# Kernel optimization log

Measured on AMD Instinct MI355X. Metric: run time of the kernel, lower is better.

The kernel has to match this reference:

```python
import jax, jax.numpy as jnp
import numpy as np

N = 100_000          # nodes
E = 1_600_000        # directed edges (avg degree 16)
H = 128              # hidden_dim
OUT = 5              # output_dim (actions)
FOV = 11             # input_dim -> image side
LIN_IN = (FOV - 2) ** 2 * 3  # 243
LN_EPS = 1e-5


def _conv2d(x, w, b):
    # x: [N,3,h,w], w: [3,3,3,3] OIHW, VALID, stride 1
    y = jax.lax.conv_general_dilated(
        x, w, window_strides=(1, 1), padding='VALID',
        dimension_numbers=('NCHW', 'OIHW', 'NCHW'))
    return y + b[None, :, None, None]


def setup_inputs() -> dict:
    key = jax.random.key(0)
    ks = jax.random.split(key, 32)
    r = lambda i, shape, s=0.05: (jax.random.normal(ks[i], shape, jnp.float32) * s)
    inp = {
        'x': jax.random.normal(ks[0], (N, 3, FOV, FOV), jnp.float32),
        'edge_index': jax.random.randint(ks[1], (2, E), 0, N, jnp.int64)
                      if jax.config.jax_enable_x64 else
                      jax.random.randint(ks[1], (2, E), 0, N, jnp.int32),
        # CustomConv params
        'conv_w': r(2, (3, 3, 3, 3)), 'conv_b': r(3, (3,)),
        'conv_self_w': r(4, (3, 3, 3, 3)), 'conv_self_b': r(5, (3,)),
        'lin_w': r(6, (LIN_IN, H)), 'lin_b': r(7, (H,)),
        'lin_self_w': r(8, (LIN_IN, H)), 'lin_self_b': r(9, (H,)),
        # 3 SAGEConv layers: lin_l (aggregated, with bias), lin_r (root, no bias)
        'sage_lw': r(10, (3, H, H)), 'sage_lb': r(11, (3, H)),
        'sage_rw': r(12, (3, H, H)),
        # LayerNorms applied after layers 0,1,2
        'ln_g': jnp.ones((3, H), jnp.float32), 'ln_b': jnp.zeros((3, H), jnp.float32),
        # post_mp MLP (dropout is identity in eval)
        'mlp_w1': r(13, (H, H)), 'mlp_b1': r(14, (H,)),
        'mlp_w2': r(15, (H, OUT)), 'mlp_b2': r(16, (OUT,)),
    }
    return inp


def _layernorm(h, g, b):
    mu = jnp.mean(h, axis=-1, keepdims=True)
    var = jnp.var(h, axis=-1, keepdims=True)
    return (h - mu) * jax.lax.rsqrt(var + LN_EPS) * g + b


def reference(x, edge_index, conv_w, conv_b, conv_self_w, conv_self_b,
              lin_w, lin_b, lin_self_w, lin_self_b,
              sage_lw, sage_lb, sage_rw, ln_g, ln_b,
              mlp_w1, mlp_b1, mlp_w2, mlp_b2):
    src, dst = edge_index[0], edge_index[1]
    valid = (src != dst)  # remove_self_loops (CustomConv only)

    # ---- layer 0: CustomConv (add aggregation) ----
    self_x = jax.nn.relu(_conv2d(x, conv_self_w, conv_self_b).reshape(N, -1))
    self_x = self_x @ lin_self_w + lin_self_b              # [N,H]
    xn = jax.nn.relu(_conv2d(x, conv_w, conv_b).reshape(N, -1))
    xn = xn @ lin_w + lin_b                                # [N,H]
    msgs = xn[src] * valid[:, None].astype(xn.dtype)       # gather + mask self loops
    h = self_x + jax.ops.segment_sum(msgs, dst, num_segments=N)

    # SAGE mean-degree counts (all edges; SAGE does not remove self loops)
    cnt = jnp.maximum(
        jax.ops.segment_sum(jnp.ones((E,), h.dtype), dst, num_segments=N), 1.0)

    emb = h
    for i in range(4):
        if i > 0:
            j = i - 1
            agg = jax.ops.segment_sum(h[src], dst, num_segments=N) / cnt[:, None]
            h = agg @ sage_lw[j] + sage_lb[j] + h @ sage_rw[j]
        emb = h
        h = jax.nn.relu(h)            # dropout p=0.25 is identity in eval
        if i != 3:
            h = _layernorm(h, ln_g[i], ln_b[i])

    # task == 'node': no pooling
    logits = (h @ mlp_w1 + mlp_b1) @ mlp_w2 + mlp_b2
    return emb, jax.nn.log_softmax(logits, axis=1)
```

## Files before the change

kernel.cpp:

```cpp
#include <hip/hip_runtime.h>
#include <hip/hip_bf16.h>

typedef __hip_bfloat16 bf16;
typedef __attribute__((ext_vector_type(8))) short v8s;
typedef __attribute__((ext_vector_type(4))) float v4f;

#define N_NODES 100000
#define N_EDGES 1600000
#define LN_EPS 1e-5f

#define OFF_CONV_W      0
#define OFF_CONV_B      81
#define OFF_CONV_SW     84
#define OFF_CONV_SB     165
#define OFF_LIN_W       168
#define OFF_LIN_B       31272
#define OFF_LIN_SW      31400
#define OFF_LIN_SB      62504
#define OFF_SAGE_LW     62632
#define OFF_SAGE_LB     111784
#define OFF_SAGE_RW     112168
#define OFF_LN_G        161320
#define OFF_LN_B        161704
#define OFF_MLP_W1      162088
#define OFF_MLP_B1      178472
#define OFF_MLP_W2      178600
#define OFF_MLP_B2      179240
#define PARAM_TOTAL     179245

#define WTL_N 65536
#define WTS_N 98304
#define WTM_N 16384

__device__ __forceinline__ unsigned short f2b(float f) {
    bf16 h = __float2bfloat16(f);
    return __builtin_bit_cast(unsigned short, h);
}
__device__ __forceinline__ float blo(unsigned u) { return __uint_as_float(u << 16); }
__device__ __forceinline__ float bhi(unsigned u) { return __uint_as_float(u & 0xffff0000u); }
__device__ __forceinline__ unsigned pack2(float lo, float hi) {
    return (unsigned)f2b(lo) | ((unsigned)f2b(hi) << 16);
}

struct Ptr17 { const void* p[17]; };

__global__ void detect_kernel(const unsigned short* __restrict__ xw,
                              const unsigned int* __restrict__ ew,
                              int* __restrict__ flags) {
    __shared__ int sawBigExp, sawHigh;
    if (threadIdx.x == 0) { sawBigExp = 0; sawHigh = 0; }
    __syncthreads();
    int localBig = 0, localHigh = 0;
    for (int i = threadIdx.x; i < 65536; i += 256) {
        unsigned e = (xw[i] >> 7) & 0xFF;
        if (e >= 0xF0) localBig = 1;
    }
    for (int i = threadIdx.x; i < 8192; i += 256) {
        if (ew[2 * i + 1] != 0) localHigh = 1;
    }
    if (localBig) atomicOr(&sawBigExp, 1);
    if (localHigh) atomicOr(&sawHigh, 1);
    __syncthreads();
    if (threadIdx.x == 0) { flags[0] = sawBigExp; flags[1] = sawHigh ? 0 : 1; }
}

__global__ void cvt_params_kernel(Ptr17 ptrs, const int* __restrict__ flags,
                                  float* __restrict__ dst) {
    int i = blockIdx.x * 256 + threadIdx.x;
    if (i >= PARAM_TOTAL) return;
    const int ksz[17] = {81,3,81,3,31104,128,31104,128,49152,384,49152,384,384,16384,128,640,5};
    int seg = 0, off = i;
    while (off >= ksz[seg]) { off -= ksz[seg]; ++seg; }
    float v;
    if (flags[0]) v = ((const float*)ptrs.p[seg])[off];
    else          v = __bfloat162float(((const bf16*)ptrs.p[seg])[off]);
    dst[i] = v;
}

__global__ void cvt2_kernel(const float* __restrict__ P,
                            unsigned short* __restrict__ wtl,
                            unsigned short* __restrict__ wts,
                            unsigned short* __restrict__ wtm) {
    int i = blockIdx.x * 256 + threadIdx.x;
    if (i < WTL_N) {
        int f = i >> 8, k = i & 255;
        float v = 0.f;
        if (k < 243) v = (f < 128) ? P[OFF_LIN_W + k * 128 + f]
                                   : P[OFF_LIN_SW + k * 128 + (f - 128)];
        wtl[i] = f2b(v);
    } else if (i < WTL_N + WTS_N) {
        int j = i - WTL_N; int l = j >> 15; int r = j & 32767; int f = r >> 8; int k = r & 255;
        float v = (k < 128) ? P[OFF_SAGE_LW + l * 16384 + k * 128 + f]
                            : P[OFF_SAGE_RW + l * 16384 + (k - 128) * 128 + f];
        wts[j] = f2b(v);
    } else if (i < WTL_N + WTS_N + WTM_N) {
        int j = i - WTL_N - WTS_N; int f = j >> 7, k = j & 127;
        wtm[j] = f2b(P[OFF_MLP_W1 + k * 128 + f]);
    }
}

__global__ __launch_bounds__(320) void conv_lin_kernel(
    const void* __restrict__ x, const float* __restrict__ P,
    const unsigned short* __restrict__ wtl, const int* __restrict__ flags,
    unsigned short* __restrict__ xnb, float* __restrict__ selfh)
{
    __shared__ unsigned short xs[5808];
    __shared__ unsigned short ysb[16][2][256];
    __shared__ float wc[2][81];
    __shared__ float bc[2][3];
    int tid = threadIdx.x;
    int n0 = blockIdx.x * 16;

    if (tid < 81) { wc[0][tid] = P[OFF_CONV_W + tid]; wc[1][tid] = P[OFF_CONV_SW + tid]; }
    else if (tid < 84) { int o = tid - 81; bc[0][o] = P[OFF_CONV_B + o]; bc[1][o] = P[OFF_CONV_SB + o]; }

    for (int i = tid; i < 416; i += 320) {
        int j = i / 26, r2 = i % 26, p = r2 / 13, k = 243 + (r2 % 13);
        ysb[j][p][k] = 0;
    }

    if (flags[0]) {
        const float* xf = (const float*)x + (size_t)n0 * 363;
        for (int i = tid; i < 5808; i += 320) xs[i] = f2b(xf[i]);
    } else {
        const uint4* xsrc = (const uint4*)((const unsigned short*)x + (size_t)n0 * 363);
        uint4* xd = (uint4*)xs;
        for (int i = tid; i < 726; i += 320) xd[i] = xsrc[i];
    }
    __syncthreads();

    if (tid < 288) {
        int j = tid / 18, rem = tid % 18;
        int p = rem / 9, oi = rem % 9;
        float acc[27];
        #pragma unroll
        for (int o = 0; o < 3; o++) {
            float b = bc[p][o];
            #pragma unroll
            for (int oj = 0; oj < 9; oj++) acc[o * 9 + oj] = b;
        }
        #pragma unroll
        for (int c = 0; c < 3; c++) {
            #pragma unroll
            for (int ki = 0; ki < 3; ki++) {
                float xr[11];
                const unsigned short* row = &xs[j * 363 + c * 121 + (oi + ki) * 11];
                #pragma unroll
                for (int t = 0; t < 11; t++) xr[t] = blo(row[t]);
                #pragma unroll
                for (int o = 0; o < 3; o++) {
                    int wb = o * 27 + c * 9 + ki * 3;
                    float w0 = wc[p][wb], w1 = wc[p][wb + 1], w2 = wc[p][wb + 2];
                    #pragma unroll
                    for (int oj = 0; oj < 9; oj++)
                        acc[o * 9 + oj] += xr[oj] * w0 + xr[oj + 1] * w1 + xr[oj + 2] * w2;
                }
            }
        }
        #pragma unroll
        for (int o = 0; o < 3; o++)
            #pragma unroll
            for (int oj = 0; oj < 9; oj++)
                ysb[j][p][o * 81 + oi * 9 + oj] = f2b(fmaxf(acc[o * 9 + oj], 0.f));
    }
    __syncthreads();

    int wave = tid >> 6, lane = tid & 63, quad = lane >> 4, col = lane & 15;
    if (wave < 4) {
        int p = wave >> 1;
        v4f acc[4];
        #pragma unroll
        for (int t = 0; t < 4; t++) { acc[t][0] = 0.f; acc[t][1] = 0.f; acc[t][2] = 0.f; acc[t][3] = 0.f; }
        for (int s = 0; s < 8; s++) {
            int kq = s * 32 + quad * 8;
            v8s a = *(const v8s*)&ysb[col][p][kq];
            #pragma unroll
            for (int t = 0; t < 4; t++) {
                int f = (wave * 4 + t) * 16 + col;
                v8s b = *(const v8s*)&wtl[(size_t)f * 256 + kq];
                acc[t] = __builtin_amdgcn_mfma_f32_16x16x32_bf16(a, b, acc[t], 0, 0, 0);
            }
        }
        #pragma unroll
        for (int t = 0; t < 4; t++) {
            int f = (wave * 4 + t) * 16 + col;
            #pragma unroll
            for (int r = 0; r < 4; r++) {
                int node = n0 + quad * 4 + r;
                float v = acc[t][r];
                if (p == 0) xnb[(size_t)node * 128 + f] = f2b(v + P[OFF_LIN_B + f]);
                else        selfh[(size_t)node * 128 + (f - 128)] = v + P[OFF_LIN_SB + (f - 128)];
            }
        }
    }
}

__device__ __forceinline__ int ld_edge(const int* __restrict__ ew, size_t elem, int isi64) {
    size_t idx = isi64 ? (elem * 2) : elem;
    return ew[idx];
}

__global__ void degree_kernel(const int* __restrict__ ew, const int* __restrict__ flags,
                              int* __restrict__ deg) {
    int e = blockIdx.x * blockDim.x + threadIdx.x;
    if (e < N_EDGES) {
        int d = ld_edge(ew, (size_t)N_EDGES + e, flags[1]);
        if ((unsigned)d < N_NODES) atomicAdd(&deg[d], 1);
    }
}

__global__ __launch_bounds__(1024) void scanA(const int* __restrict__ deg, int* __restrict__ rowptr,
                                              float* __restrict__ cntf, int* __restrict__ bsum) {
    __shared__ int s[1024];
    int tid = threadIdx.x;
    int i = blockIdx.x * 1024 + tid;
    int v = (i < N_NODES) ? deg[i] : 0;
    s[tid] = v;
    __syncthreads();
    for (int off = 1; off < 1024; off <<= 1) {
        int t = (tid >= off) ? s[tid - off] : 0;
        __syncthreads();
        s[tid] += t;
        __syncthreads();
    }
    if (i < N_NODES) {
        rowptr[i] = s[tid] - v;
        cntf[i] = (float)(v < 1 ? 1 : v);
    }
    if (tid == 1023) bsum[blockIdx.x] = s[1023];
}

__global__ void scanB(const int* __restrict__ bsum, int* __restrict__ boff, int nb, int* __restrict__ rowptr_end) {
    if (threadIdx.x == 0 && blockIdx.x == 0) {
        int run = 0;
        for (int i = 0; i < nb; i++) { boff[i] = run; run += bsum[i]; }
        *rowptr_end = run;
    }
}

__global__ __launch_bounds__(1024) void scanC(int* __restrict__ rowptr, const int* __restrict__ boff,
                                              int* __restrict__ cursor) {
    int i = blockIdx.x * 1024 + threadIdx.x;
    if (i < N_NODES) {
        int v = rowptr[i] + boff[blockIdx.x];
        rowptr[i] = v;
        cursor[i] = v;
    }
}

__global__ void fill_kernel(const int* __restrict__ ew, const int* __restrict__ flags,
                            int* __restrict__ cursor, int* __restrict__ csr) {
    int e = blockIdx.x * blockDim.x + threadIdx.x;
    if (e < N_EDGES) {
        int isi64 = flags[1];
        int s = ld_edge(ew, (size_t)e, isi64);
        int d = ld_edge(ew, (size_t)N_EDGES + e, isi64);
        if ((unsigned)d < N_NODES) {
            int p = atomicAdd(&cursor[d], 1);
            if ((unsigned)p < N_EDGES)
                csr[p] = ((unsigned)s < N_NODES) ? (s | ((s == d) ? (int)0x80000000 : 0)) : -1;
        }
    }
}

__global__ __launch_bounds__(256) void agg0ln_kernel(const unsigned short* __restrict__ xnb,
        const float* __restrict__ selfh, const int* __restrict__ rowptr, const int* __restrict__ csr,
        const float* __restrict__ lng, const float* __restrict__ lnb,
        unsigned short* __restrict__ zb) {
    int wave = threadIdx.x >> 6, lane = threadIdx.x & 63;
    int g = lane >> 4, c = lane & 15;
    int n = blockIdx.x * 4 + wave;
    int beg = rowptr[n], end = rowptr[n + 1];
    float a[8];
    #pragma unroll
    for (int i = 0; i < 8; i++) a[i] = 0.f;
    const uint4* x4 = (const uint4*)xnb;
    for (int b = beg; b < end; b += 64) {
        int bl = b + lane;
        int my = (bl < end) ? csr[bl] : -1;
        int nb = end - b; if (nb > 64) nb = 64;
        for (int i = 0; i < nb; i += 16) {
            int sv0 = __shfl(my, i + g, 64);
            int sv1 = __shfl(my, i + 4 + g, 64);
            int sv2 = __shfl(my, i + 8 + g, 64);
            int sv3 = __shfl(my, i + 12 + g, 64);
            bool va0 = ((unsigned)sv0 < N_NODES);
            bool va1 = ((unsigned)sv1 < N_NODES);
            bool va2 = ((unsigned)sv2 < N_NODES);
            bool va3 = ((unsigned)sv3 < N_NODES);
            uint4 v0 = x4[(size_t)(va0 ? sv0 : 0) * 16 + c];
            uint4 v1 = x4[(size_t)(va1 ? sv1 : 0) * 16 + c];
            uint4 v2 = x4[(size_t)(va2 ? sv2 : 0) * 16 + c];
            uint4 v3 = x4[(size_t)(va3 ? sv3 : 0) * 16 + c];
            if (va0) {
                a[0] += blo(v0.x); a[1] += bhi(v0.x);
                a[2] += blo(v0.y); a[3] += bhi(v0.y);
                a[4] += blo(v0.z); a[5] += bhi(v0.z);
                a[6] += blo(v0.w); a[7] += bhi(v0.w);
            }
            if (va1) {
                a[0] += blo(v1.x); a[1] += bhi(v1.x);
                a[2] += blo(v1.y); a[3] += bhi(v1.y);
                a[4] += blo(v1.z); a[5] += bhi(v1.z);
                a[6] += blo(v1.w); a[7] += bhi(v1.w);
            }
            if (va2) {
                a[0] += blo(v2.x); a[1] += bhi(v2.x);
                a[2] += blo(v2.y); a[3] += bhi(v2.y);
                a[4] += blo(v2.z); a[5] += bhi(v2.z);
                a[6] += blo(v2.w); a[7] += bhi(v2.w);
            }
            if (va3) {
                a[0] += blo(v3.x); a[1] += bhi(v3.x);
                a[2] += blo(v3.y); a[3] += bhi(v3.y);
                a[4] += blo(v3.z); a[5] += bhi(v3.z);
                a[6] += blo(v3.w); a[7] += bhi(v3.w);
            }
        }
    }
    #pragma unroll
    for (int i = 0; i < 8; i++) {
        a[i] += __shfl_xor(a[i], 16, 64);
        a[i] += __shfl_xor(a[i], 32, 64);
    }
    if (g == 0) {
        const float4* s4 = (const float4*)(selfh + (size_t)n * 128 + c * 8);
        float4 s0 = s4[0], s1 = s4[1];
        float v[8];
        v[0] = s0.x + a[0]; v[1] = s0.y + a[1]; v[2] = s0.z + a[2]; v[3] = s0.w + a[3];
        v[4] = s1.x + a[4]; v[5] = s1.y + a[5]; v[6] = s1.z + a[6]; v[7] = s1.w + a[7];
        float s = 0.f, sq = 0.f;
        #pragma unroll
        for (int i = 0; i < 8; i++) {
            v[i] = fmaxf(v[i], 0.f);
            s += v[i]; sq += v[i] * v[i];
        }
        #pragma unroll
        for (int m = 8; m >= 1; m >>= 1) {
            s  += __shfl_xor(s, m, 64);
            sq += __shfl_xor(sq, m, 64);
        }
        float mu = s * (1.f / 128.f);
        float var = sq * (1.f / 128.f) - mu * mu;
        float is = rsqrtf(var + LN_EPS);
        const float4* g4 = (const float4*)(lng + c * 8);
        const float4* b4 = (const float4*)(lnb + c * 8);
        float4 g0 = g4[0], g1 = g4[1], b0 = b4[0], b1 = b4[1];
        float z[8];
        z[0] = (v[0] - mu) * is * g0.x + b0.x; z[1] = (v[1] - mu) * is * g0.y + b0.y;
        z[2] = (v[2] - mu) * is * g0.z + b0.z; z[3] = (v[3] - mu) * is * g0.w + b0.w;
        z[4] = (v[4] - mu) * is * g1.x + b1.x; z[5] = (v[5] - mu) * is * g1.y + b1.y;
        z[6] = (v[6] - mu) * is * g1.z + b1.z; z[7] = (v[7] - mu) * is * g1.w + b1.w;
        uint4 o;
        o.x = pack2(z[0], z[1]); o.y = pack2(z[2], z[3]);
        o.z = pack2(z[4], z[5]); o.w = pack2(z[6], z[7]);
        ((uint4*)zb)[(size_t)n * 16 + c] = o;
    }
}

__global__ __launch_bounds__(256) void aggm_kernel(const unsigned short* __restrict__ zb,
        const int* __restrict__ rowptr, const int* __restrict__ csr,
        const float* __restrict__ cntf, unsigned short* __restrict__ aggb) {
    int wave = threadIdx.x >> 6, lane = threadIdx.x & 63;
    int g = lane >> 4, c = lane & 15;
    int n = blockIdx.x * 4 + wave;
    int beg = rowptr[n], end = rowptr[n + 1];
    float a[8];
    #pragma unroll
    for (int i = 0; i < 8; i++) a[i] = 0.f;
    const uint4* z4 = (const uint4*)zb;
    for (int b = beg; b < end; b += 64) {
        int bl = b + lane;
        int my = (bl < end) ? csr[bl] : -1;
        int nb = end - b; if (nb > 64) nb = 64;
        for (int i = 0; i < nb; i += 16) {
            int sv0 = __shfl(my, i + g, 64) & 0x7fffffff;
            int sv1 = __shfl(my, i + 4 + g, 64) & 0x7fffffff;
            int sv2 = __shfl(my, i + 8 + g, 64) & 0x7fffffff;
            int sv3 = __shfl(my, i + 12 + g, 64) & 0x7fffffff;
            bool va0 = (sv0 < N_NODES);
            bool va1 = (sv1 < N_NODES);
            bool va2 = (sv2 < N_NODES);
            bool va3 = (sv3 < N_NODES);
            uint4 v0 = z4[(size_t)(va0 ? sv0 : 0) * 16 + c];
            uint4 v1 = z4[(size_t)(va1 ? sv1 : 0) * 16 + c];
            uint4 v2 = z4[(size_t)(va2 ? sv2 : 0) * 16 + c];
            uint4 v3 = z4[(size_t)(va3 ? sv3 : 0) * 16 + c];
            if (va0) {
                a[0] += blo(v0.x); a[1] += bhi(v0.x);
                a[2] += blo(v0.y); a[3] += bhi(v0.y);
                a[4] += blo(v0.z); a[5] += bhi(v0.z);
                a[6] += blo(v0.w); a[7] += bhi(v0.w);
            }
            if (va1) {
                a[0] += blo(v1.x); a[1] += bhi(v1.x);
                a[2] += blo(v1.y); a[3] += bhi(v1.y);
                a[4] += blo(v1.z); a[5] += bhi(v1.z);
                a[6] += blo(v1.w); a[7] += bhi(v1.w);
            }
            if (va2) {
                a[0] += blo(v2.x); a[1] += bhi(v2.x);
                a[2] += blo(v2.y); a[3] += bhi(v2.y);
                a[4] += blo(v2.z); a[5] += bhi(v2.z);
                a[6] += blo(v2.w); a[7] += bhi(v2.w);
            }
            if (va3) {
                a[0] += blo(v3.x); a[1] += bhi(v3.x);
                a[2] += blo(v3.y); a[3] += bhi(v3.y);
                a[4] += blo(v3.z); a[5] += bhi(v3.z);
                a[6] += blo(v3.w); a[7] += bhi(v3.w);
            }
        }
    }
    #pragma unroll
    for (int i = 0; i < 8; i++) {
        a[i] += __shfl_xor(a[i], 16, 64);
        a[i] += __shfl_xor(a[i], 32, 64);
    }
    if (g == 0) {
        float inv = 1.f / cntf[n];
        uint4 o;
        o.x = pack2(a[0] * inv, a[1] * inv); o.y = pack2(a[2] * inv, a[3] * inv);
        o.z = pack2(a[4] * inv, a[5] * inv); o.w = pack2(a[6] * inv, a[7] * inv);
        ((uint4*)aggb)[(size_t)n * 16 + c] = o;
    }
}

__global__ __launch_bounds__(256) void sageln_kernel(const unsigned short* __restrict__ aggb,
        unsigned short* __restrict__ zb, const unsigned short* __restrict__ wts,
        const float* __restrict__ lb, const float* __restrict__ lng, const float* __restrict__ lnb,
        int last, float* __restrict__ hout) {
    __shared__ float hb[16][128];
    int tid = threadIdx.x;
    int n0 = blockIdx.x * 16;
    int wave = tid >> 6, lane = tid & 63, quad = lane >> 4, col = lane & 15;
    int nodeA = n0 + col;

    v4f acc[2];
    #pragma unroll
    for (int t = 0; t < 2; t++) { acc[t][0] = 0.f; acc[t][1] = 0.f; acc[t][2] = 0.f; acc[t][3] = 0.f; }
    #pragma unroll
    for (int s = 0; s < 8; s++) {
        int kq = s * 32 + quad * 8;
        const unsigned short* abase = (s < 4) ? (aggb + (size_t)nodeA * 128 + kq)
                                              : (zb + (size_t)nodeA * 128 + (kq - 128));
        v8s a = *(const v8s*)abase;
        #pragma unroll
        for (int t = 0; t < 2; t++) {
            int f = (wave * 2 + t) * 16 + col;
            v8s b = *(const v8s*)&wts[(size_t)f * 256 + kq];
            acc[t] = __builtin_amdgcn_mfma_f32_16x16x32_bf16(a, b, acc[t], 0, 0, 0);
        }
    }
    #pragma unroll
    for (int t = 0; t < 2; t++) {
        int f = (wave * 2 + t) * 16 + col;
        float bias = lb[f];
        #pragma unroll
        for (int r = 0; r < 4; r++)
            hb[quad * 4 + r][f] = acc[t][r] + bias;
    }
    __syncthreads();

    #pragma unroll
    for (int jj = 0; jj < 4; jj++) {
        int j = wave * 4 + jj;
        int node = n0 + j;
        float v0 = hb[j][2 * lane], v1 = hb[j][2 * lane + 1];
        if (last) {
            float2 w; w.x = v0; w.y = v1;
            ((float2*)hout)[(size_t)node * 64 + lane] = w;
        } else {
            float r0 = fmaxf(v0, 0.f), r1 = fmaxf(v1, 0.f);
            float s = r0 + r1, sq = r0 * r0 + r1 * r1;
            #pragma unroll
            for (int m = 32; m >= 1; m >>= 1) {
                s  += __shfl_xor(s, m, 64);
                sq += __shfl_xor(sq, m, 64);
            }
            float mu = s * (1.f / 128.f);
            float var = sq * (1.f / 128.f) - mu * mu;
            float inv = rsqrtf(var + LN_EPS);
            float z0 = (r0 - mu) * inv * lng[2 * lane]     + lnb[2 * lane];
            float z1 = (r1 - mu) * inv * lng[2 * lane + 1] + lnb[2 * lane + 1];
            ((unsigned int*)zb)[(size_t)node * 64 + lane] = pack2(z0, z1);
        }
    }
}

__global__ __launch_bounds__(256) void mlp_kernel(const float* __restrict__ h,
        const unsigned short* __restrict__ wtm, const float* __restrict__ P,
        const int* __restrict__ flags, void* __restrict__ out) {
    __shared__ unsigned short rb[16][128];
    __shared__ float mb[16][128];
    __shared__ float lg[16][5];
    int tid = threadIdx.x;
    int n0 = blockIdx.x * 16;
    int isf = flags[0];

    const float2* h2 = (const float2*)h;
    for (int i = tid; i < 16 * 64; i += 256) {
        int j = i >> 6, q = i & 63;
        float2 v = h2[(size_t)(n0 + j) * 64 + q];
        size_t oi = (size_t)(n0 + j) * 128 + 2 * q;
        if (isf) { ((float*)out)[oi] = v.x; ((float*)out)[oi + 1] = v.y; }
        else ((unsigned int*)out)[oi >> 1] = pack2(v.x, v.y);
        rb[j][2 * q]     = f2b(fmaxf(v.x, 0.f));
        rb[j][2 * q + 1] = f2b(fmaxf(v.y, 0.f));
    }
    __syncthreads();

    int wave = tid >> 6, lane = tid & 63, quad = lane >> 4, col = lane & 15;
    v4f acc[2];
    #pragma unroll
    for (int t = 0; t < 2; t++) { acc[t][0] = 0.f; acc[t][1] = 0.f; acc[t][2] = 0.f; acc[t][3] = 0.f; }
    #pragma unroll
    for (int s = 0; s < 4; s++) {
        int kq = s * 32 + quad * 8;
        v8s a = *(const v8s*)&rb[col][kq];
        #pragma unroll
        for (int t = 0; t < 2; t++) {
            int f = (wave * 2 + t) * 16 + col;
            v8s b = *(const v8s*)&wtm[(size_t)f * 128 + kq];
            acc[t] = __builtin_amdgcn_mfma_f32_16x16x32_bf16(a, b, acc[t], 0, 0, 0);
        }
    }
    #pragma unroll
    for (int t = 0; t < 2; t++) {
        int f = (wave * 2 + t) * 16 + col;
        float bias = P[OFF_MLP_B1 + f];
        #pragma unroll
        for (int r = 0; r < 4; r++)
            mb[quad * 4 + r][f] = acc[t][r] + bias;
    }
    __syncthreads();

    if (tid < 80) {
        int j = tid / 5, o = tid - (tid / 5) * 5;
        float a = P[OFF_MLP_B2 + o];
        for (int k = 0; k < 128; k++) a += mb[j][k] * P[OFF_MLP_W2 + k * 5 + o];
        lg[j][o] = a;
    }
    __syncthreads();
    if (tid < 16) {
        int j = tid;
        float mx = lg[j][0];
        #pragma unroll
        for (int o = 1; o < 5; o++) mx = fmaxf(mx, lg[j][o]);
        float se = 0.f;
        #pragma unroll
        for (int o = 0; o < 5; o++) se += expf(lg[j][o] - mx);
        float lse = mx + logf(se);
        size_t base = (size_t)N_NODES * 128 + (size_t)(n0 + j) * 5;
        #pragma unroll
        for (int o = 0; o < 5; o++) {
            float v = lg[j][o] - lse;
            if (isf) ((float*)out)[base + o] = v;
            else     ((bf16*)out)[base + o] = __float2bfloat16(v);
        }
    }
}

extern "C" void kernel_launch(void* const* d_in, const int* in_sizes, int n_in,
                              void* d_out, int out_size, void* d_ws, size_t ws_size,
                              hipStream_t stream) {
    const void* x  = d_in[0];
    const int*  ew = (const int*)d_in[1];

    Ptr17 ptrs;
    for (int i = 0; i < 17; i++) ptrs.p[i] = d_in[2 + i];

    char* w = (char*)d_ws;
    auto carve = [&](size_t bytes) { char* r = w; w += (bytes + 255) & ~(size_t)255; return r; };
    float*          bufS  = (float*)carve((size_t)N_NODES * 128 * 4);
    unsigned short* xnb   = (unsigned short*)carve((size_t)N_NODES * 128 * 2);
    unsigned short* zb    = (unsigned short*)carve((size_t)N_NODES * 128 * 2);
    unsigned short* aggb  = (unsigned short*)carve((size_t)N_NODES * 128 * 2);
    float*          pf32  = (float*)carve((size_t)PARAM_TOTAL * 4);
    unsigned short* wtl   = (unsigned short*)carve((size_t)WTL_N * 2);
    unsigned short* wts   = (unsigned short*)carve((size_t)WTS_N * 2);
    unsigned short* wtm   = (unsigned short*)carve((size_t)WTM_N * 2);
    int*   deg    = (int*)carve((size_t)N_NODES * 4);
    int*   rowptr = (int*)carve((size_t)(N_NODES + 64) * 4);
    int*   cursor = (int*)carve((size_t)N_NODES * 4);
    float* cntf   = (float*)carve((size_t)N_NODES * 4);
    int*   bsum   = (int*)carve(512);
    int*   boff   = (int*)carve(512);
    int*   flags  = (int*)carve(256);
    int*   csr    = (int*)carve((size_t)N_EDGES * 4);

    const int SCAN_BLOCKS = (N_NODES + 1023) / 1024;

    detect_kernel<<<1, 256, 0, stream>>>((const unsigned short*)x, (const unsigned int*)ew, flags);
    cvt_params_kernel<<<(PARAM_TOTAL + 255) / 256, 256, 0, stream>>>(ptrs, flags, pf32);
    cvt2_kernel<<<(WTL_N + WTS_N + WTM_N + 255) / 256, 256, 0, stream>>>(pf32, wtl, wts, wtm);

    hipMemsetAsync(deg, 0, (size_t)N_NODES * 4, stream);

    conv_lin_kernel<<<N_NODES / 16, 320, 0, stream>>>(x, pf32, wtl, flags, xnb, bufS);

    degree_kernel<<<(N_EDGES + 255) / 256, 256, 0, stream>>>(ew, flags, deg);
    scanA<<<SCAN_BLOCKS, 1024, 0, stream>>>(deg, rowptr, cntf, bsum);
    scanB<<<1, 1, 0, stream>>>(bsum, boff, SCAN_BLOCKS, rowptr + N_NODES);
    scanC<<<SCAN_BLOCKS, 1024, 0, stream>>>(rowptr, boff, cursor);
    fill_kernel<<<(N_EDGES + 255) / 256, 256, 0, stream>>>(ew, flags, cursor, csr);

    agg0ln_kernel<<<N_NODES / 4, 256, 0, stream>>>(xnb, bufS, rowptr, csr,
        pf32 + OFF_LN_G, pf32 + OFF_LN_B, zb);

    for (int l = 0; l < 3; l++) {
        aggm_kernel<<<N_NODES / 4, 256, 0, stream>>>(zb, rowptr, csr, cntf, aggb);
        sageln_kernel<<<N_NODES / 16, 256, 0, stream>>>(aggb, zb, wts + (size_t)l * 32768,
            pf32 + OFF_SAGE_LB + l * 128,
            pf32 + OFF_LN_G + (l + 1) * 128, pf32 + OFF_LN_B + (l + 1) * 128,
            (l == 2) ? 1 : 0, bufS);
    }

    mlp_kernel<<<N_NODES / 16, 256, 0, stream>>>(bufS, wtm, pf32, flags, d_out);
}
```

Baseline: 1.150 ms.

## Fuse SAGE mean-aggregation into the MFMA linear+LayerNorm kernel with ping-pong buffers

Merges the neighbor mean-aggregation kernel and the SAGE linear+LayerNorm kernel into one. Each block aggregates 16 nodes into shared memory, then feeds them straight to the MFMA. The next layer's activations go to a separate ping-pong buffer, so other blocks never see an overwritten input. This removes one launch per layer and the global write and reread of the aggregated features. In exchange, the block does its gathers serially per wave (4 nodes each) before the MFMA, and the MFMA loads now mix LDS and global reads, which could hurt latency hiding.

Result: faster. 1.087 ms (-5.5%).

```diff
diff --git a/kernel.cpp b/kernel.cpp
--- a/kernel.cpp
+++ b/kernel.cpp
@@ -358,92 +358,95 @@
     }
 }
 
-__global__ __launch_bounds__(256) void aggm_kernel(const unsigned short* __restrict__ zb,
+__global__ __launch_bounds__(256) void sagefused_kernel(
+        const unsigned short* __restrict__ cur,
         const int* __restrict__ rowptr, const int* __restrict__ csr,
-        const float* __restrict__ cntf, unsigned short* __restrict__ aggb) {
-    int wave = threadIdx.x >> 6, lane = threadIdx.x & 63;
-    int g = lane >> 4, c = lane & 15;
-    int n = blockIdx.x * 4 + wave;
-    int beg = rowptr[n], end = rowptr[n + 1];
-    float a[8];
-    #pragma unroll
-    for (int i = 0; i < 8; i++) a[i] = 0.f;
-    const uint4* z4 = (const uint4*)zb;
-    for (int b = beg; b < end; b += 64) {
-        int bl = b + lane;
-        int my = (bl < end) ? csr[bl] : -1;
-        int nb = end - b; if (nb > 64) nb = 64;
-        for (int i = 0; i < nb; i += 16) {
-            int sv0 = __shfl(my, i + g, 64) & 0x7fffffff;
-            int sv1 = __shfl(my, i + 4 + g, 64) & 0x7fffffff;
-            int sv2 = __shfl(my, i + 8 + g, 64) & 0x7fffffff;
-            int sv3 = __shfl(my, i + 12 + g, 64) & 0x7fffffff;
-            bool va0 = (sv0 < N_NODES);
-            bool va1 = (sv1 < N_NODES);
-            bool va2 = (sv2 < N_NODES);
-            bool va3 = (sv3 < N_NODES);
-            uint4 v0 = z4[(size_t)(va0 ? sv0 : 0) * 16 + c];
-            uint4 v1 = z4[(size_t)(va1 ? sv1 : 0) * 16 + c];
-            uint4 v2 = z4[(size_t)(va2 ? sv2 : 0) * 16 + c];
-            uint4 v3 = z4[(size_t)(va3 ? sv3 : 0) * 16 + c];
-            if (va0) {
-                a[0] += blo(v0.x); a[1] += bhi(v0.x);
-                a[2] += blo(v0.y); a[3] += bhi(v0.y);
-                a[4] += blo(v0.z); a[5] += bhi(v0.z);
-                a[6] += blo(v0.w); a[7] += bhi(v0.w);
-            }
-            if (va1) {
-                a[0] += blo(v1.x); a[1] += bhi(v1.x);
-                a[2] += blo(v1.y); a[3] += bhi(v1.y);
-                a[4] += blo(v1.z); a[5] += bhi(v1.z);
-                a[6] += blo(v1.w); a[7] += bhi(v1.w);
-            }
-            if (va2) {
-                a[0] += blo(v2.x); a[1] += bhi(v2.x);
-                a[2] += blo(v2.y); a[3] += bhi(v2.y);
-                a[4] += blo(v2.z); a[5] += bhi(v2.z);
-                a[6] += blo(v2.w); a[7] += bhi(v2.w);
-            }
-            if (va3) {
-                a[0] += blo(v3.x); a[1] += bhi(v3.x);
-                a[2] += blo(v3.y); a[3] += bhi(v3.y);
-                a[4] += blo(v3.z); a[5] += bhi(v3.z);
-                a[6] += blo(v3.w); a[7] += bhi(v3.w);
-            }
-        }
-    }
-    #pragma unroll
-    for (int i = 0; i < 8; i++) {
-        a[i] += __shfl_xor(a[i], 16, 64);
-        a[i] += __shfl_xor(a[i], 32, 64);
-    }
-    if (g == 0) {
-        float inv = 1.f / cntf[n];
-        uint4 o;
-        o.x = pack2(a[0] * inv, a[1] * inv); o.y = pack2(a[2] * inv, a[3] * inv);
-        o.z = pack2(a[4] * inv, a[5] * inv); o.w = pack2(a[6] * inv, a[7] * inv);
-        ((uint4*)aggb)[(size_t)n * 16 + c] = o;
-    }
-}
-
-__global__ __launch_bounds__(256) void sageln_kernel(const unsigned short* __restrict__ aggb,
-        unsigned short* __restrict__ zb, const unsigned short* __restrict__ wts,
+        const float* __restrict__ cntf, const unsigned short* __restrict__ wts,
         const float* __restrict__ lb, const float* __restrict__ lng, const float* __restrict__ lnb,
-        int last, float* __restrict__ hout) {
+        int last, unsigned short* __restrict__ nxt, float* __restrict__ hout) {
+    __shared__ unsigned short al[16][128];
     __shared__ float hb[16][128];
     int tid = threadIdx.x;
     int n0 = blockIdx.x * 16;
-    int wave = tid >> 6, lane = tid & 63, quad = lane >> 4, col = lane & 15;
+    int wave = tid >> 6, lane = tid & 63;
+    int g = lane >> 4, c = lane & 15;
+    const uint4* z4 = (const uint4*)cur;
+
+    for (int q = 0; q < 4; q++) {
+        int jj = wave * 4 + q;
+        int n = n0 + jj;
+        int beg = rowptr[n], end = rowptr[n + 1];
+        float a[8];
+        #pragma unroll
+        for (int i = 0; i < 8; i++) a[i] = 0.f;
+        for (int b = beg; b < end; b += 64) {
+            int bl = b + lane;
+            int my = (bl < end) ? csr[bl] : -1;
+            int nb = end - b; if (nb > 64) nb = 64;
+            for (int i = 0; i < nb; i += 16) {
+                int sv0 = __shfl(my, i + g, 64) & 0x7fffffff;
+                int sv1 = __shfl(my, i + 4 + g, 64) & 0x7fffffff;
+                int sv2 = __shfl(my, i + 8 + g, 64) & 0x7fffffff;
+                int sv3 = __shfl(my, i + 12 + g, 64) & 0x7fffffff;
+                bool va0 = (sv0 < N_NODES);
+                bool va1 = (sv1 < N_NODES);
+                bool va2 = (sv2 < N_NODES);
+                bool va3 = (sv3 < N_NODES);
+                uint4 v0 = z4[(size_t)(va0 ? sv0 : 0) * 16 + c];
+                uint4 v1 = z4[(size_t)(va1 ? sv1 : 0) * 16 + c];
+                uint4 v2 = z4[(size_t)(va2 ? sv2 : 0) * 16 + c];
+                uint4 v3 = z4[(size_t)(va3 ? sv3 : 0) * 16 + c];
+                if (va0) {
+                    a[0] += blo(v0.x); a[1] += bhi(v0.x);
+                    a[2] += blo(v0.y); a[3] += bhi(v0.y);
+                    a[4] += blo(v0.z); a[5] += bhi(v0.z);
+                    a[6] += blo(v0.w); a[7] += bhi(v0.w);
+                }
+                if (va1) {
+                    a[0] += blo(v1.x); a[1] += bhi(v1.x);
+                    a[2] += blo(v1.y); a[3] += bhi(v1.y);
+                    a[4] += blo(v1.z); a[5] += bhi(v1.z);
+                    a[6] += blo(v1.w); a[7] += bhi(v1.w);
+                }
+                if (va2) {
+                    a[0] += blo(v2.x); a[1] += bhi(v2.x);
+                    a[2] += blo(v2.y); a[3] += bhi(v2.y);
+                    a[4] += blo(v2.z); a[5] += bhi(v2.z);
+                    a[6] += blo(v2.w); a[7] += bhi(v2.w);
+                }
+                if (va3) {
+                    a[0] += blo(v3.x); a[1] += bhi(v3.x);
+                    a[2] += blo(v3.y); a[3] += bhi(v3.y);
+                    a[4] += blo(v3.z); a[5] += bhi(v3.z);
+                    a[6] += blo(v3.w); a[7] += bhi(v3.w);
+                }
+            }
+        }
+        #pragma unroll
+        for (int i = 0; i < 8; i++) {
+            a[i] += __shfl_xor(a[i], 16, 64);
+            a[i] += __shfl_xor(a[i], 32, 64);
+        }
+        if (g == 0) {
+            float inv = 1.f / cntf[n];
+            uint4 o;
+            o.x = pack2(a[0] * inv, a[1] * inv); o.y = pack2(a[2] * inv, a[3] * inv);
+            o.z = pack2(a[4] * inv, a[5] * inv); o.w = pack2(a[6] * inv, a[7] * inv);
+            ((uint4*)&al[jj][0])[c] = o;
+        }
+    }
+    __syncthreads();
+
+    int quad = g, col = c;
     int nodeA = n0 + col;
-
     v4f acc[2];
     #pragma unroll
     for (int t = 0; t < 2; t++) { acc[t][0] = 0.f; acc[t][1] = 0.f; acc[t][2] = 0.f; acc[t][3] = 0.f; }
     #pragma unroll
     for (int s = 0; s < 8; s++) {
         int kq = s * 32 + quad * 8;
-        const unsigned short* abase = (s < 4) ? (aggb + (size_t)nodeA * 128 + kq)
-                                              : (zb + (size_t)nodeA * 128 + (kq - 128));
+        const unsigned short* abase = (s < 4) ? &al[col][kq]
+                                              : (cur + (size_t)nodeA * 128 + (kq - 128));
         v8s a = *(const v8s*)abase;
         #pragma unroll
         for (int t = 0; t < 2; t++) {
@@ -483,7 +486,7 @@
             float inv = rsqrtf(var + LN_EPS);
             float z0 = (r0 - mu) * inv * lng[2 * lane]     + lnb[2 * lane];
             float z1 = (r1 - mu) * inv * lng[2 * lane + 1] + lnb[2 * lane + 1];
-            ((unsigned int*)zb)[(size_t)node * 64 + lane] = pack2(z0, z1);
+            ((unsigned int*)nxt)[(size_t)node * 64 + lane] = pack2(z0, z1);
         }
     }
 }
@@ -608,12 +611,15 @@
     agg0ln_kernel<<<N_NODES / 4, 256, 0, stream>>>(xnb, bufS, rowptr, csr,
         pf32 + OFF_LN_G, pf32 + OFF_LN_B, zb);
 
+    unsigned short* cur = zb;
+    unsigned short* nxt = aggb;
     for (int l = 0; l < 3; l++) {
-        aggm_kernel<<<N_NODES / 4, 256, 0, stream>>>(zb, rowptr, csr, cntf, aggb);
-        sageln_kernel<<<N_NODES / 16, 256, 0, stream>>>(aggb, zb, wts + (size_t)l * 32768,
+        sagefused_kernel<<<N_NODES / 16, 256, 0, stream>>>(cur, rowptr, csr, cntf,
+            wts + (size_t)l * 32768,
             pf32 + OFF_SAGE_LB + l * 128,
             pf32 + OFF_LN_G + (l + 1) * 128, pf32 + OFF_LN_B + (l + 1) * 128,
-            (l == 2) ? 1 : 0, bufS);
+            (l == 2) ? 1 : 0, nxt, bufS);
+        unsigned short* t = cur; cur = nxt; nxt = t;
     }
 
     mlp_kernel<<<N_NODES / 16, 256, 0, stream>>>(bufS, wtm, pf32, flags, d_out);
```
